# Optimization experiments

Hardware: AMD Instinct MI355X
Metric: run time of the kernel (lower is better)

## Reference

```python
import jax, jax.numpy as jnp
from jax import lax
import numpy as np

T, B, I, H = 512, 1024, 64, 64


def setup_inputs() -> dict:
    key = jax.random.key(0)
    k1, k2, k3, k4, k5 = jax.random.split(key, 5)
    s = 1.0 / np.sqrt(H)  # PyTorch GRU init scale
    X = jax.random.normal(k1, (T, B, I), dtype=jnp.float32)
    W_ih = jax.random.uniform(k2, (3 * H, I), jnp.float32, -s, s)
    W_hh = jax.random.uniform(k3, (3 * H, H), jnp.float32, -s, s)
    b_ih = jax.random.uniform(k4, (3 * H,), jnp.float32, -s, s)
    b_hh = jax.random.uniform(k5, (3 * H,), jnp.float32, -s, s)
    return {"X": X, "W_ih": W_ih, "W_hh": W_hh, "b_ih": b_ih, "b_hh": b_hh}


def reference(X, W_ih, W_hh, b_ih, b_hh):
    # Single-layer GRU, PyTorch semantics, gate order (r, z, n), h0 = 0.
    Hh = W_hh.shape[1]
    # Precompute input-side gate projections for all timesteps: [T, B, 3H]
    gates_x = jnp.einsum('tbi,gi->tbg', X, W_ih) + b_ih

    def step(h, gx):
        gh = h @ W_hh.T + b_hh  # [B, 3H]
        r = jax.nn.sigmoid(gx[:, :Hh] + gh[:, :Hh])
        z = jax.nn.sigmoid(gx[:, Hh:2 * Hh] + gh[:, Hh:2 * Hh])
        n = jnp.tanh(gx[:, 2 * Hh:] + r * gh[:, 2 * Hh:])
        h_new = (1.0 - z) * n + z * h
        return h_new, h_new

    h0 = jnp.zeros((X.shape[1], Hh), dtype=X.dtype)
    h_last, output = lax.scan(step, h0, gates_x)
    return output, h_last[None]  # ([T,B,H], [1,B,H])
```

## Files before the change

### kernel.cpp

```cpp
#include <hip/hip_runtime.h>


typedef _Float16 half8 __attribute__((ext_vector_type(8)));
typedef float    f32x4 __attribute__((ext_vector_type(4)));

#define T_STEPS 512
#define BATCH   1024

struct XBuf { float4 a0, a1, b0, b1; };

__device__ __forceinline__ half8 cvt8(const float4& a, const float4& b) {
    half8 h;
    h[0] = (_Float16)a.x; h[1] = (_Float16)a.y; h[2] = (_Float16)a.z; h[3] = (_Float16)a.w;
    h[4] = (_Float16)b.x; h[5] = (_Float16)b.y; h[6] = (_Float16)b.z; h[7] = (_Float16)b.w;
    return h;
}

__device__ __forceinline__ half8 loadw8(const float* p) {
    const float4* q = (const float4*)p;
    float4 a = q[0], b = q[1];
    return cvt8(a, b);
}

__device__ __forceinline__ void block_sync() {
    asm volatile("s_waitcnt lgkmcnt(0)" ::: "memory");
    __builtin_amdgcn_s_barrier();
    asm volatile("" ::: "memory");
}

#define MFMA16(A, B, C) __builtin_amdgcn_mfma_f32_16x16x32_f16((A), (B), (C), 0, 0, 0)

__global__ __launch_bounds__(256, 1)
void gru_mfma_kernel(const float* __restrict__ X,
                     const float* __restrict__ W_ih,
                     const float* __restrict__ W_hh,
                     const float* __restrict__ b_ih,
                     const float* __restrict__ b_hh,
                     float* __restrict__ out)
{
    const int tid   = threadIdx.x;
    const int w     = tid >> 6;
    const int l     = tid & 63;
    const int c     = l & 15;
    const int g4    = l >> 4;
    const int u     = w * 16 + c;
    const int row   = c;
    const int brow0 = blockIdx.x * 16;

    __shared__ __align__(16) _Float16 hbuf[2][16][72];

    const half8 Br0 = loadw8(W_ih + (u)       * 64 +  0 + 8 * g4);
    const half8 Br1 = loadw8(W_ih + (u)       * 64 + 32 + 8 * g4);
    const half8 Br2 = loadw8(W_hh + (u)       * 64 +  0 + 8 * g4);
    const half8 Br3 = loadw8(W_hh + (u)       * 64 + 32 + 8 * g4);
    const half8 Bz0 = loadw8(W_ih + (64 + u)  * 64 +  0 + 8 * g4);
    const half8 Bz1 = loadw8(W_ih + (64 + u)  * 64 + 32 + 8 * g4);
    const half8 Bz2 = loadw8(W_hh + (64 + u)  * 64 +  0 + 8 * g4);
    const half8 Bz3 = loadw8(W_hh + (64 + u)  * 64 + 32 + 8 * g4);
    const half8 Bnx0 = loadw8(W_ih + (128 + u) * 64 +  0 + 8 * g4);
    const half8 Bnx1 = loadw8(W_ih + (128 + u) * 64 + 32 + 8 * g4);
    const half8 Bnh0 = loadw8(W_hh + (128 + u) * 64 +  0 + 8 * g4);
    const half8 Bnh1 = loadw8(W_hh + (128 + u) * 64 + 32 + 8 * g4);

    const float rb  = b_ih[u]        + b_hh[u];
    const float zb  = b_ih[64 + u]   + b_hh[64 + u];
    const float nxb = b_ih[128 + u];
    const float nhb = b_hh[128 + u];

    f32x4 hp = {0.f, 0.f, 0.f, 0.f};

#define ISSUE_X(XB, T) do {                                                   \
        const float* px_ = X + ((T) * BATCH + brow0 + row) * 64 + 8 * g4;     \
        (XB).a0 = ((const float4*)px_)[0];                                    \
        (XB).a1 = ((const float4*)px_)[1];                                    \
        const float* py_ = px_ + 32;                                          \
        (XB).b0 = ((const float4*)py_)[0];                                    \
        (XB).b1 = ((const float4*)py_)[1];                                    \
    } while (0)

    XBuf xb0, xb1;
    ISSUE_X(xb0, 0);
    ISSUE_X(xb1, 1);

    for (int k = tid; k < 16 * 72; k += 256)
        ((_Float16*)hbuf)[k] = (_Float16)0.f;
    __syncthreads();

#define STEP(T, XB) do {                                                      \
        const int p_ = (T) & 1;                                               \
        const half8 hf0 = *(const half8*)&hbuf[p_][row][8 * g4];              \
        const half8 hf1 = *(const half8*)&hbuf[p_][row][32 + 8 * g4];         \
        const half8 xf0 = cvt8((XB).a0, (XB).a1);                             \
        const half8 xf1 = cvt8((XB).b0, (XB).b1);                             \
        { int tn_ = (T) + 2; if (tn_ > T_STEPS - 1) tn_ = T_STEPS - 1;        \
          ISSUE_X(XB, tn_); }                                                 \
        f32x4 cr  = {rb, rb, rb, rb};                                         \
        f32x4 cz  = {zb, zb, zb, zb};                                         \
        f32x4 cnx = {nxb, nxb, nxb, nxb};                                     \
        f32x4 cnh = {nhb, nhb, nhb, nhb};                                     \
        cr  = MFMA16(xf0, Br0, cr);   cr  = MFMA16(xf1, Br1, cr);             \
        cz  = MFMA16(xf0, Bz0, cz);   cz  = MFMA16(xf1, Bz1, cz);             \
        cnx = MFMA16(xf0, Bnx0, cnx); cnx = MFMA16(xf1, Bnx1, cnx);           \
        cr  = MFMA16(hf0, Br2, cr);   cr  = MFMA16(hf1, Br3, cr);             \
        cz  = MFMA16(hf0, Bz2, cz);   cz  = MFMA16(hf1, Bz3, cz);             \
        cnh = MFMA16(hf0, Bnh0, cnh); cnh = MFMA16(hf1, Bnh1, cnh);           \
        _Pragma("unroll")                                                     \
        for (int i = 0; i < 4; ++i) {                                         \
            const float rv = __builtin_amdgcn_rcpf(1.f + __expf(-cr[i]));     \
            const float zv = __builtin_amdgcn_rcpf(1.f + __expf(-cz[i]));     \
            const float npre = fmaf(rv, cnh[i], cnx[i]);                      \
            const float nv =                                                  \
                1.f - 2.f * __builtin_amdgcn_rcpf(1.f + __expf(2.f * npre));  \
            const float hn = fmaf(zv, hp[i] - nv, nv);                        \
            hp[i] = hn;                                                       \
            hbuf[p_ ^ 1][4 * g4 + i][u] = (_Float16)hn;                       \
            out[((T) * BATCH + brow0 + 4 * g4 + i) * 64 + u] = hn;            \
        }                                                                     \
        block_sync();                                                         \
    } while (0)

    #pragma unroll 1
    for (int t = 0; t < T_STEPS; t += 2) {
        STEP(t, xb0);
        STEP(t + 1, xb1);
    }

    #pragma unroll
    for (int i = 0; i < 4; ++i)
        out[T_STEPS * BATCH * 64 + (brow0 + 4 * g4 + i) * 64 + u] = hp[i];

#undef STEP
#undef ISSUE_X
}

extern "C" void kernel_launch(void* const* d_in, const int* in_sizes, int n_in,
                              void* d_out, int out_size, void* d_ws, size_t ws_size,
                              hipStream_t stream) {
    const float* X    = (const float*)d_in[0];
    const float* W_ih = (const float*)d_in[1];
    const float* W_hh = (const float*)d_in[2];
    const float* b_ih = (const float*)d_in[3];
    const float* b_hh = (const float*)d_in[4];
    float* out = (float*)d_out;

    dim3 grid(BATCH / 16);
    dim3 block(256);
    gru_mfma_kernel<<<grid, block, 0, stream>>>(X, W_ih, W_hh, b_ih, b_hh, out);
}
```

Baseline: 344.5 us.

## Software-pipeline input projection one step ahead of recurrent MFMA chain

The input-side gate MFMAs for timestep t+1 are now computed during step t, before the hidden-state MFMAs. This takes them off the serial h-dependent critical path, so each step only waits on six recurrent MFMAs plus the activation math. The next step's X tile is now converted one step earlier, which leaves less time to hide its global-load latency. It also keeps three more accumulator vectors live across the barrier.

Measured after the change: 438.9 us. 27.4% more time.

```diff
diff --git a/kernel.cpp b/kernel.cpp
--- a/kernel.cpp
+++ b/kernel.cpp
@@ -49,14 +49,14 @@
 
     __shared__ __align__(16) _Float16 hbuf[2][16][72];
 
-    const half8 Br0 = loadw8(W_ih + (u)       * 64 +  0 + 8 * g4);
-    const half8 Br1 = loadw8(W_ih + (u)       * 64 + 32 + 8 * g4);
-    const half8 Br2 = loadw8(W_hh + (u)       * 64 +  0 + 8 * g4);
-    const half8 Br3 = loadw8(W_hh + (u)       * 64 + 32 + 8 * g4);
-    const half8 Bz0 = loadw8(W_ih + (64 + u)  * 64 +  0 + 8 * g4);
-    const half8 Bz1 = loadw8(W_ih + (64 + u)  * 64 + 32 + 8 * g4);
-    const half8 Bz2 = loadw8(W_hh + (64 + u)  * 64 +  0 + 8 * g4);
-    const half8 Bz3 = loadw8(W_hh + (64 + u)  * 64 + 32 + 8 * g4);
+    const half8 Brx0 = loadw8(W_ih + (u)       * 64 +  0 + 8 * g4);
+    const half8 Brx1 = loadw8(W_ih + (u)       * 64 + 32 + 8 * g4);
+    const half8 Brh0 = loadw8(W_hh + (u)       * 64 +  0 + 8 * g4);
+    const half8 Brh1 = loadw8(W_hh + (u)       * 64 + 32 + 8 * g4);
+    const half8 Bzx0 = loadw8(W_ih + (64 + u)  * 64 +  0 + 8 * g4);
+    const half8 Bzx1 = loadw8(W_ih + (64 + u)  * 64 + 32 + 8 * g4);
+    const half8 Bzh0 = loadw8(W_hh + (64 + u)  * 64 +  0 + 8 * g4);
+    const half8 Bzh1 = loadw8(W_hh + (64 + u)  * 64 + 32 + 8 * g4);
     const half8 Bnx0 = loadw8(W_ih + (128 + u) * 64 +  0 + 8 * g4);
     const half8 Bnx1 = loadw8(W_ih + (128 + u) * 64 + 32 + 8 * g4);
     const half8 Bnh0 = loadw8(W_hh + (128 + u) * 64 +  0 + 8 * g4);
@@ -82,33 +82,51 @@
     ISSUE_X(xb0, 0);
     ISSUE_X(xb1, 1);
 
-    for (int k = tid; k < 16 * 72; k += 256)
+    for (int k = tid; k < 2 * 16 * 72; k += 256)
         ((_Float16*)hbuf)[k] = (_Float16)0.f;
+
+    f32x4 axr = {rb, rb, rb, rb};
+    f32x4 axz = {zb, zb, zb, zb};
+    f32x4 axn = {nxb, nxb, nxb, nxb};
+    {
+        const half8 x0 = cvt8(xb0.a0, xb0.a1);
+        const half8 x1 = cvt8(xb0.b0, xb0.b1);
+        axr = MFMA16(x0, Brx0, axr); axr = MFMA16(x1, Brx1, axr);
+        axz = MFMA16(x0, Bzx0, axz); axz = MFMA16(x1, Bzx1, axz);
+        axn = MFMA16(x0, Bnx0, axn); axn = MFMA16(x1, Bnx1, axn);
+    }
     __syncthreads();
 
-#define STEP(T, XB) do {                                                      \
+#define STEP(T, XA, XB) do {                                                  \
         const int p_ = (T) & 1;                                               \
+                 \
         const half8 hf0 = *(const half8*)&hbuf[p_][row][8 * g4];              \
         const half8 hf1 = *(const half8*)&hbuf[p_][row][32 + 8 * g4];         \
-        const half8 xf0 = cvt8((XB).a0, (XB).a1);                             \
-        const half8 xf1 = cvt8((XB).b0, (XB).b1);                             \
+           \
+        const half8 nxf0 = cvt8((XB).a0, (XB).a1);                            \
+        const half8 nxf1 = cvt8((XB).b0, (XB).b1);                            \
+        f32x4 naxr = {rb, rb, rb, rb};                                        \
+        f32x4 naxz = {zb, zb, zb, zb};                                        \
+        f32x4 naxn = {nxb, nxb, nxb, nxb};                                    \
+        naxr = MFMA16(nxf0, Brx0, naxr); naxr = MFMA16(nxf1, Brx1, naxr);     \
+        naxz = MFMA16(nxf0, Bzx0, naxz); naxz = MFMA16(nxf1, Bzx1, naxz);     \
+        naxn = MFMA16(nxf0, Bnx0, naxn); naxn = MFMA16(nxf1, Bnx1, naxn);     \
         { int tn_ = (T) + 2; if (tn_ > T_STEPS - 1) tn_ = T_STEPS - 1;        \
-          ISSUE_X(XB, tn_); }                                                 \
-        f32x4 cr  = {rb, rb, rb, rb};                                         \
-        f32x4 cz  = {zb, zb, zb, zb};                                         \
-        f32x4 cnx = {nxb, nxb, nxb, nxb};                                     \
-        f32x4 cnh = {nhb, nhb, nhb, nhb};                                     \
-        cr  = MFMA16(xf0, Br0, cr);   cr  = MFMA16(xf1, Br1, cr);             \
-        cz  = MFMA16(xf0, Bz0, cz);   cz  = MFMA16(xf1, Bz1, cz);             \
-        cnx = MFMA16(xf0, Bnx0, cnx); cnx = MFMA16(xf1, Bnx1, cnx);           \
-        cr  = MFMA16(hf0, Br2, cr);   cr  = MFMA16(hf1, Br3, cr);             \
-        cz  = MFMA16(hf0, Bz2, cz);   cz  = MFMA16(hf1, Bz3, cz);             \
-        cnh = MFMA16(hf0, Bnh0, cnh); cnh = MFMA16(hf1, Bnh1, cnh);           \
+          ISSUE_X(XA, tn_); }                                                 \
+                             \
+        f32x4 hr  = {0.f, 0.f, 0.f, 0.f};                                     \
+        f32x4 hz  = {0.f, 0.f, 0.f, 0.f};                                     \
+        f32x4 hnh = {nhb, nhb, nhb, nhb};                                     \
+        hr  = MFMA16(hf0, Brh0, hr);   hr  = MFMA16(hf1, Brh1, hr);           \
+        hz  = MFMA16(hf0, Bzh0, hz);   hz  = MFMA16(hf1, Bzh1, hz);           \
+        hnh = MFMA16(hf0, Bnh0, hnh);  hnh = MFMA16(hf1, Bnh1, hnh);          \
         _Pragma("unroll")                                                     \
         for (int i = 0; i < 4; ++i) {                                         \
-            const float rv = __builtin_amdgcn_rcpf(1.f + __expf(-cr[i]));     \
-            const float zv = __builtin_amdgcn_rcpf(1.f + __expf(-cz[i]));     \
-            const float npre = fmaf(rv, cnh[i], cnx[i]);                      \
+            const float crv = axr[i] + hr[i];                                 \
+            const float czv = axz[i] + hz[i];                                 \
+            const float rv = __builtin_amdgcn_rcpf(1.f + __expf(-crv));       \
+            const float zv = __builtin_amdgcn_rcpf(1.f + __expf(-czv));       \
+            const float npre = fmaf(rv, hnh[i], axn[i]);                      \
             const float nv =                                                  \
                 1.f - 2.f * __builtin_amdgcn_rcpf(1.f + __expf(2.f * npre));  \
             const float hn = fmaf(zv, hp[i] - nv, nv);                        \
@@ -116,13 +134,14 @@
             hbuf[p_ ^ 1][4 * g4 + i][u] = (_Float16)hn;                       \
             out[((T) * BATCH + brow0 + 4 * g4 + i) * 64 + u] = hn;            \
         }                                                                     \
+        axr = naxr; axz = naxz; axn = naxn;                                   \
         block_sync();                                                         \
     } while (0)
 
     #pragma unroll 1
     for (int t = 0; t < T_STEPS; t += 2) {
-        STEP(t, xb0);
-        STEP(t + 1, xb1);
+        STEP(t, xb0, xb1);
+        STEP(t + 1, xb1, xb0);
     }
 
     #pragma unroll
```

## Run each batch tile's GRU recurrence in one wave using cross-lane permutes

Applied to the files above, without the earlier changes.

Each 16-row batch tile is now handled by a single 64-lane wave instead of four waves. The hidden state is exchanged through ds_bpermute register shuffles rather than an LDS buffer and a block barrier at every timestep. The MFMA operands are swapped so the weights act as the A operand, and outputs are written as float4 vectors. This removes the per-step workgroup barrier and LDS round-trip. In exchange, each wave holds all 48 weight fragments in registers, issues four times as many MFMAs serially per step, and only 64 single-wave blocks run on the GPU.

Result: slower. 766.7 us (+122.6%).

```diff
diff --git a/kernel.cpp b/kernel.cpp
--- a/kernel.cpp
+++ b/kernel.cpp
@@ -1,8 +1,10 @@
 #include <hip/hip_runtime.h>
 
 
-typedef _Float16 half8 __attribute__((ext_vector_type(8)));
-typedef float    f32x4 __attribute__((ext_vector_type(4)));
+typedef _Float16 half8  __attribute__((ext_vector_type(8)));
+typedef __fp16   fp16x2 __attribute__((ext_vector_type(2)));
+typedef float    f32x4  __attribute__((ext_vector_type(4)));
+typedef int      i32x4  __attribute__((ext_vector_type(4)));
 
 #define T_STEPS 512
 #define BATCH   1024
@@ -18,116 +20,151 @@
 
 __device__ __forceinline__ half8 loadw8(const float* p) {
     const float4* q = (const float4*)p;
-    float4 a = q[0], b = q[1];
-    return cvt8(a, b);
+    return cvt8(q[0], q[1]);
 }
 
-__device__ __forceinline__ void block_sync() {
-    asm volatile("s_waitcnt lgkmcnt(0)" ::: "memory");
-    __builtin_amdgcn_s_barrier();
-    asm volatile("" ::: "memory");
+__device__ __forceinline__ int packrtz(float x, float y) {
+    fp16x2 p = __builtin_amdgcn_cvt_pkrtz(x, y);
+    return __builtin_bit_cast(int, p);
 }
 
 #define MFMA16(A, B, C) __builtin_amdgcn_mfma_f32_16x16x32_f16((A), (B), (C), 0, 0, 0)
 
-__global__ __launch_bounds__(256, 1)
-void gru_mfma_kernel(const float* __restrict__ X,
-                     const float* __restrict__ W_ih,
-                     const float* __restrict__ W_hh,
-                     const float* __restrict__ b_ih,
-                     const float* __restrict__ b_hh,
-                     float* __restrict__ out)
+__global__ __launch_bounds__(64, 1)
+void gru_1wave_kernel(const float* __restrict__ X,
+                      const float* __restrict__ W_ih,
+                      const float* __restrict__ W_hh,
+                      const float* __restrict__ b_ih,
+                      const float* __restrict__ b_hh,
+                      float* __restrict__ out)
 {
-    const int tid   = threadIdx.x;
-    const int w     = tid >> 6;
-    const int l     = tid & 63;
-    const int c     = l & 15;
+    const int l     = threadIdx.x;
+    const int b     = l & 15;
     const int g4    = l >> 4;
-    const int u     = w * 16 + c;
-    const int row   = c;
     const int brow0 = blockIdx.x * 16;
+    const bool hiHalf = (l >= 32);
 
-    __shared__ __align__(16) _Float16 hbuf[2][16][72];
+    const int idx0 = (b + 16 * ((g4 & 1) << 1)) << 2;
+    const int idx1 = idx0 + 64;
 
-    const half8 Br0 = loadw8(W_ih + (u)       * 64 +  0 + 8 * g4);
-    const half8 Br1 = loadw8(W_ih + (u)       * 64 + 32 + 8 * g4);
-    const half8 Br2 = loadw8(W_hh + (u)       * 64 +  0 + 8 * g4);
-    const half8 Br3 = loadw8(W_hh + (u)       * 64 + 32 + 8 * g4);
-    const half8 Bz0 = loadw8(W_ih + (64 + u)  * 64 +  0 + 8 * g4);
-    const half8 Bz1 = loadw8(W_ih + (64 + u)  * 64 + 32 + 8 * g4);
-    const half8 Bz2 = loadw8(W_hh + (64 + u)  * 64 +  0 + 8 * g4);
-    const half8 Bz3 = loadw8(W_hh + (64 + u)  * 64 + 32 + 8 * g4);
-    const half8 Bnx0 = loadw8(W_ih + (128 + u) * 64 +  0 + 8 * g4);
-    const half8 Bnx1 = loadw8(W_ih + (128 + u) * 64 + 32 + 8 * g4);
-    const half8 Bnh0 = loadw8(W_hh + (128 + u) * 64 +  0 + 8 * g4);
-    const half8 Bnh1 = loadw8(W_hh + (128 + u) * 64 + 32 + 8 * g4);
+    half8 Wih[3][4][2], Whh[3][4][2];
+    #pragma unroll
+    for (int g = 0; g < 3; ++g)
+        #pragma unroll
+        for (int ut = 0; ut < 4; ++ut)
+            #pragma unroll
+            for (int kk = 0; kk < 2; ++kk) {
+                const int row = g * 64 + 16 * ut + b;
+                Wih[g][ut][kk] = loadw8(W_ih + row * 64 + 32 * kk + 8 * g4);
+                Whh[g][ut][kk] = loadw8(W_hh + row * 64 + 32 * kk + 8 * g4);
+            }
 
-    const float rb  = b_ih[u]        + b_hh[u];
-    const float zb  = b_ih[64 + u]   + b_hh[64 + u];
-    const float nxb = b_ih[128 + u];
-    const float nhb = b_hh[128 + u];
+    f32x4 bR[4], bZ[4], bNX[4], bNH[4];
+    #pragma unroll
+    for (int ut = 0; ut < 4; ++ut) {
+        const int o = 16 * ut + 4 * g4;
+        const float4 i0 = *(const float4*)(b_ih + o);
+        const float4 h0 = *(const float4*)(b_hh + o);
+        const float4 i1 = *(const float4*)(b_ih + 64 + o);
+        const float4 h1 = *(const float4*)(b_hh + 64 + o);
+        const float4 i2 = *(const float4*)(b_ih + 128 + o);
+        const float4 h2 = *(const float4*)(b_hh + 128 + o);
+        bR[ut][0] = i0.x + h0.x; bR[ut][1] = i0.y + h0.y;
+        bR[ut][2] = i0.z + h0.z; bR[ut][3] = i0.w + h0.w;
+        bZ[ut][0] = i1.x + h1.x; bZ[ut][1] = i1.y + h1.y;
+        bZ[ut][2] = i1.z + h1.z; bZ[ut][3] = i1.w + h1.w;
+        bNX[ut][0] = i2.x; bNX[ut][1] = i2.y; bNX[ut][2] = i2.z; bNX[ut][3] = i2.w;
+        bNH[ut][0] = h2.x; bNH[ut][1] = h2.y; bNH[ut][2] = h2.z; bNH[ut][3] = h2.w;
+    }
 
-    f32x4 hp = {0.f, 0.f, 0.f, 0.f};
+    f32x4 hp[4] = {{0.f,0.f,0.f,0.f},{0.f,0.f,0.f,0.f},
+                   {0.f,0.f,0.f,0.f},{0.f,0.f,0.f,0.f}};
+    int hh[4][2] = {{0,0},{0,0},{0,0},{0,0}};
 
 #define ISSUE_X(XB, T) do {                                                   \
-        const float* px_ = X + ((T) * BATCH + brow0 + row) * 64 + 8 * g4;     \
+        const float* px_ = X + ((T) * BATCH + brow0 + b) * 64 + 8 * g4;       \
         (XB).a0 = ((const float4*)px_)[0];                                    \
         (XB).a1 = ((const float4*)px_)[1];                                    \
-        const float* py_ = px_ + 32;                                          \
-        (XB).b0 = ((const float4*)py_)[0];                                    \
-        (XB).b1 = ((const float4*)py_)[1];                                    \
+        (XB).b0 = ((const float4*)(px_ + 32))[0];                             \
+        (XB).b1 = ((const float4*)(px_ + 32))[1];                             \
     } while (0)
 
     XBuf xb0, xb1;
     ISSUE_X(xb0, 0);
     ISSUE_X(xb1, 1);
 
-    for (int k = tid; k < 16 * 72; k += 256)
-        ((_Float16*)hbuf)[k] = (_Float16)0.f;
-    __syncthreads();
-
-#define STEP(T, XB) do {                                                      \
-        const int p_ = (T) & 1;                                               \
-        const half8 hf0 = *(const half8*)&hbuf[p_][row][8 * g4];              \
-        const half8 hf1 = *(const half8*)&hbuf[p_][row][32 + 8 * g4];         \
-        const half8 xf0 = cvt8((XB).a0, (XB).a1);                             \
-        const half8 xf1 = cvt8((XB).b0, (XB).b1);                             \
+#define STEP(T, XA) do {                                                      \
+           \
+        i32x4 f0v, f1v;                                                       \
+        _Pragma("unroll")                                                     \
+        for (int jp = 0; jp < 4; ++jp) {                                      \
+            const int idx_ = (jp < 2) ? idx0 : idx1;                          \
+            const int lo0 = __builtin_amdgcn_ds_bpermute(idx_, hh[0][jp & 1]);\
+            const int hi0 = __builtin_amdgcn_ds_bpermute(idx_, hh[1][jp & 1]);\
+            const int lo1 = __builtin_amdgcn_ds_bpermute(idx_, hh[2][jp & 1]);\
+            const int hi1 = __builtin_amdgcn_ds_bpermute(idx_, hh[3][jp & 1]);\
+            f0v[jp] = hiHalf ? hi0 : lo0;                                     \
+            f1v[jp] = hiHalf ? hi1 : lo1;                                     \
+        }                                                                     \
+        const half8 Fh0 = __builtin_bit_cast(half8, f0v);                     \
+        const half8 Fh1 = __builtin_bit_cast(half8, f1v);                     \
+                         \
+        const half8 xf0 = cvt8((XA).a0, (XA).a1);                             \
+        const half8 xf1 = cvt8((XA).b0, (XA).b1);                             \
         { int tn_ = (T) + 2; if (tn_ > T_STEPS - 1) tn_ = T_STEPS - 1;        \
-          ISSUE_X(XB, tn_); }                                                 \
-        f32x4 cr  = {rb, rb, rb, rb};                                         \
-        f32x4 cz  = {zb, zb, zb, zb};                                         \
-        f32x4 cnx = {nxb, nxb, nxb, nxb};                                     \
-        f32x4 cnh = {nhb, nhb, nhb, nhb};                                     \
-        cr  = MFMA16(xf0, Br0, cr);   cr  = MFMA16(xf1, Br1, cr);             \
-        cz  = MFMA16(xf0, Bz0, cz);   cz  = MFMA16(xf1, Bz1, cz);             \
-        cnx = MFMA16(xf0, Bnx0, cnx); cnx = MFMA16(xf1, Bnx1, cnx);           \
-        cr  = MFMA16(hf0, Br2, cr);   cr  = MFMA16(hf1, Br3, cr);             \
-        cz  = MFMA16(hf0, Bz2, cz);   cz  = MFMA16(hf1, Bz3, cz);             \
-        cnh = MFMA16(hf0, Bnh0, cnh); cnh = MFMA16(hf1, Bnh1, cnh);           \
+          ISSUE_X(XA, tn_); }                                                 \
+            \
+        f32x4 aR[4], aZ[4], aNX[4], aNH[4];                                   \
         _Pragma("unroll")                                                     \
-        for (int i = 0; i < 4; ++i) {                                         \
-            const float rv = __builtin_amdgcn_rcpf(1.f + __expf(-cr[i]));     \
-            const float zv = __builtin_amdgcn_rcpf(1.f + __expf(-cz[i]));     \
-            const float npre = fmaf(rv, cnh[i], cnx[i]);                      \
-            const float nv =                                                  \
-                1.f - 2.f * __builtin_amdgcn_rcpf(1.f + __expf(2.f * npre));  \
-            const float hn = fmaf(zv, hp[i] - nv, nv);                        \
-            hp[i] = hn;                                                       \
-            hbuf[p_ ^ 1][4 * g4 + i][u] = (_Float16)hn;                       \
-            out[((T) * BATCH + brow0 + 4 * g4 + i) * 64 + u] = hn;            \
+        for (int ut = 0; ut < 4; ++ut) {                                      \
+            aR[ut]  = MFMA16(Wih[0][ut][0], xf0, bR[ut]);                     \
+            aR[ut]  = MFMA16(Wih[0][ut][1], xf1, aR[ut]);                     \
+            aZ[ut]  = MFMA16(Wih[1][ut][0], xf0, bZ[ut]);                     \
+            aZ[ut]  = MFMA16(Wih[1][ut][1], xf1, aZ[ut]);                     \
+            aNX[ut] = MFMA16(Wih[2][ut][0], xf0, bNX[ut]);                    \
+            aNX[ut] = MFMA16(Wih[2][ut][1], xf1, aNX[ut]);                    \
         }                                                                     \
-        block_sync();                                                         \
+        _Pragma("unroll")                                                     \
+        for (int ut = 0; ut < 4; ++ut) {                                      \
+            aR[ut]  = MFMA16(Whh[0][ut][0], Fh0, aR[ut]);                     \
+            aR[ut]  = MFMA16(Whh[0][ut][1], Fh1, aR[ut]);                     \
+            aZ[ut]  = MFMA16(Whh[1][ut][0], Fh0, aZ[ut]);                     \
+            aZ[ut]  = MFMA16(Whh[1][ut][1], Fh1, aZ[ut]);                     \
+            aNH[ut] = MFMA16(Whh[2][ut][0], Fh0, bNH[ut]);                    \
+            aNH[ut] = MFMA16(Whh[2][ut][1], Fh1, aNH[ut]);                    \
+        }                                                                     \
+                             \
+        _Pragma("unroll")                                                     \
+        for (int ut = 0; ut < 4; ++ut) {                                      \
+            f32x4 hn4;                                                        \
+            _Pragma("unroll")                                                 \
+            for (int i = 0; i < 4; ++i) {                                     \
+                const float rv = __builtin_amdgcn_rcpf(1.f + __expf(-aR[ut][i]));  \
+                const float zv = __builtin_amdgcn_rcpf(1.f + __expf(-aZ[ut][i]));  \
+                const float npre = fmaf(rv, aNH[ut][i], aNX[ut][i]);          \
+                const float nv =                                              \
+                    1.f - 2.f * __builtin_amdgcn_rcpf(1.f + __expf(2.f * npre));   \
+                const float hn = fmaf(zv, hp[ut][i] - nv, nv);                \
+                hp[ut][i] = hn;                                               \
+                hn4[i] = hn;                                                  \
+            }                                                                 \
+            hh[ut][0] = packrtz(hn4[0], hn4[1]);                              \
+            hh[ut][1] = packrtz(hn4[2], hn4[3]);                              \
+            *(f32x4*)(out + ((T) * BATCH + brow0 + b) * 64                    \
+                          + 16 * ut + 4 * g4) = hn4;                          \
+        }                                                                     \
     } while (0)
 
     #pragma unroll 1
     for (int t = 0; t < T_STEPS; t += 2) {
-        STEP(t, xb0);
+        STEP(t,     xb0);
         STEP(t + 1, xb1);
     }
 
     #pragma unroll
-    for (int i = 0; i < 4; ++i)
-        out[T_STEPS * BATCH * 64 + (brow0 + 4 * g4 + i) * 64 + u] = hp[i];
+    for (int ut = 0; ut < 4; ++ut)
+        *(f32x4*)(out + T_STEPS * BATCH * 64 + (brow0 + b) * 64
+                      + 16 * ut + 4 * g4) = hp[ut];
 
 #undef STEP
 #undef ISSUE_X
@@ -144,6 +181,6 @@
     float* out = (float*)d_out;
 
     dim3 grid(BATCH / 16);
-    dim3 block(256);
-    gru_mfma_kernel<<<grid, block, 0, stream>>>(X, W_ih, W_hh, b_ih, b_hh, out);
+    dim3 block(64);
+    gru_1wave_kernel<<<grid, block, 0, stream>>>(X, W_ih, W_hh, b_ih, b_hh, out);
 }
```

## Pair two batch tiles per block and fold exp scaling into weights

Applied to the files above, without the earlier changes.

Each block now runs two independent 16-row batch tiles across 8 waves, which halves the grid to 32 blocks of 512 threads. The log2e and negation factors are folded into the fp16 weights and biases so the gate activations use exp2 directly and skip a multiply. Activation conversion switches to packed cvt_pkrtz instructions. The cost is that both tiles share one block-wide barrier per step, the grid uses fewer CUs, and baking the scale into fp16 weights adds some rounding error.

New measurement: 652.5 us. 1.89x slower.

```diff
diff --git a/kernel.cpp b/kernel.cpp
--- a/kernel.cpp
+++ b/kernel.cpp
@@ -1,25 +1,38 @@
 #include <hip/hip_runtime.h>
 
 
-typedef _Float16 half8 __attribute__((ext_vector_type(8)));
-typedef float    f32x4 __attribute__((ext_vector_type(4)));
+typedef _Float16 half8  __attribute__((ext_vector_type(8)));
+typedef __fp16   fp16x2 __attribute__((ext_vector_type(2)));
+typedef float    f32x4  __attribute__((ext_vector_type(4)));
+typedef int      i32x4  __attribute__((ext_vector_type(4)));
 
 #define T_STEPS 512
 #define BATCH   1024
+#define LOG2E   1.4426950408889634f
 
 struct XBuf { float4 a0, a1, b0, b1; };
 
-__device__ __forceinline__ half8 cvt8(const float4& a, const float4& b) {
+__device__ __forceinline__ int pk2(float x, float y) {
+    fp16x2 p = __builtin_amdgcn_cvt_pkrtz(x, y);
+    return __builtin_bit_cast(int, p);
+}
+
+__device__ __forceinline__ half8 cvt8p(const float4& a, const float4& b) {
+    i32x4 v;
+    v[0] = pk2(a.x, a.y); v[1] = pk2(a.z, a.w);
+    v[2] = pk2(b.x, b.y); v[3] = pk2(b.z, b.w);
+    return __builtin_bit_cast(half8, v);
+}
+
+__device__ __forceinline__ half8 loadw8s(const float* p, float s) {
+    const float4* q = (const float4*)p;
+    float4 a = q[0], b = q[1];
+    a.x *= s; a.y *= s; a.z *= s; a.w *= s;
+    b.x *= s; b.y *= s; b.z *= s; b.w *= s;
     half8 h;
     h[0] = (_Float16)a.x; h[1] = (_Float16)a.y; h[2] = (_Float16)a.z; h[3] = (_Float16)a.w;
     h[4] = (_Float16)b.x; h[5] = (_Float16)b.y; h[6] = (_Float16)b.z; h[7] = (_Float16)b.w;
     return h;
-}
-
-__device__ __forceinline__ half8 loadw8(const float* p) {
-    const float4* q = (const float4*)p;
-    float4 a = q[0], b = q[1];
-    return cvt8(a, b);
 }
 
 __device__ __forceinline__ void block_sync() {
@@ -30,8 +43,8 @@
 
 #define MFMA16(A, B, C) __builtin_amdgcn_mfma_f32_16x16x32_f16((A), (B), (C), 0, 0, 0)
 
-__global__ __launch_bounds__(256, 1)
-void gru_mfma_kernel(const float* __restrict__ X,
+__global__ __launch_bounds__(512, 1)
+void gru_pair_kernel(const float* __restrict__ X,
                      const float* __restrict__ W_ih,
                      const float* __restrict__ W_hh,
                      const float* __restrict__ b_ih,
@@ -39,33 +52,38 @@
                      float* __restrict__ out)
 {
     const int tid   = threadIdx.x;
-    const int w     = tid >> 6;
+    const int wid   = tid >> 6;
+    const int wq    = wid & 3;
+    const int tile  = wid >> 2;
     const int l     = tid & 63;
     const int c     = l & 15;
     const int g4    = l >> 4;
-    const int u     = w * 16 + c;
+    const int u     = wq * 16 + c;
     const int row   = c;
-    const int brow0 = blockIdx.x * 16;
+    const int brow0 = blockIdx.x * 32 + tile * 16;
 
-    __shared__ __align__(16) _Float16 hbuf[2][16][72];
+    __shared__ __align__(16) _Float16 hbuf[2][2][16][72];
 
-    const half8 Br0 = loadw8(W_ih + (u)       * 64 +  0 + 8 * g4);
-    const half8 Br1 = loadw8(W_ih + (u)       * 64 + 32 + 8 * g4);
-    const half8 Br2 = loadw8(W_hh + (u)       * 64 +  0 + 8 * g4);
-    const half8 Br3 = loadw8(W_hh + (u)       * 64 + 32 + 8 * g4);
-    const half8 Bz0 = loadw8(W_ih + (64 + u)  * 64 +  0 + 8 * g4);
-    const half8 Bz1 = loadw8(W_ih + (64 + u)  * 64 + 32 + 8 * g4);
-    const half8 Bz2 = loadw8(W_hh + (64 + u)  * 64 +  0 + 8 * g4);
-    const half8 Bz3 = loadw8(W_hh + (64 + u)  * 64 + 32 + 8 * g4);
-    const half8 Bnx0 = loadw8(W_ih + (128 + u) * 64 +  0 + 8 * g4);
-    const half8 Bnx1 = loadw8(W_ih + (128 + u) * 64 + 32 + 8 * g4);
-    const half8 Bnh0 = loadw8(W_hh + (128 + u) * 64 +  0 + 8 * g4);
-    const half8 Bnh1 = loadw8(W_hh + (128 + u) * 64 + 32 + 8 * g4);
+    const float sRZ = -LOG2E;
+    const float sN  = 2.0f * LOG2E;
 
-    const float rb  = b_ih[u]        + b_hh[u];
-    const float zb  = b_ih[64 + u]   + b_hh[64 + u];
-    const float nxb = b_ih[128 + u];
-    const float nhb = b_hh[128 + u];
+    const half8 Brx0 = loadw8s(W_ih + (u)       * 64 +  0 + 8 * g4, sRZ);
+    const half8 Brx1 = loadw8s(W_ih + (u)       * 64 + 32 + 8 * g4, sRZ);
+    const half8 Brh0 = loadw8s(W_hh + (u)       * 64 +  0 + 8 * g4, sRZ);
+    const half8 Brh1 = loadw8s(W_hh + (u)       * 64 + 32 + 8 * g4, sRZ);
+    const half8 Bzx0 = loadw8s(W_ih + (64 + u)  * 64 +  0 + 8 * g4, sRZ);
+    const half8 Bzx1 = loadw8s(W_ih + (64 + u)  * 64 + 32 + 8 * g4, sRZ);
+    const half8 Bzh0 = loadw8s(W_hh + (64 + u)  * 64 +  0 + 8 * g4, sRZ);
+    const half8 Bzh1 = loadw8s(W_hh + (64 + u)  * 64 + 32 + 8 * g4, sRZ);
+    const half8 Bnx0 = loadw8s(W_ih + (128 + u) * 64 +  0 + 8 * g4, sN);
+    const half8 Bnx1 = loadw8s(W_ih + (128 + u) * 64 + 32 + 8 * g4, sN);
+    const half8 Bnh0 = loadw8s(W_hh + (128 + u) * 64 +  0 + 8 * g4, sN);
+    const half8 Bnh1 = loadw8s(W_hh + (128 + u) * 64 + 32 + 8 * g4, sN);
+
+    const float rb  = sRZ * (b_ih[u]      + b_hh[u]);
+    const float zb  = sRZ * (b_ih[64 + u] + b_hh[64 + u]);
+    const float nxb = sN * b_ih[128 + u];
+    const float nhb = sN * b_hh[128 + u];
 
     f32x4 hp = {0.f, 0.f, 0.f, 0.f};
 
@@ -73,47 +91,46 @@
         const float* px_ = X + ((T) * BATCH + brow0 + row) * 64 + 8 * g4;     \
         (XB).a0 = ((const float4*)px_)[0];                                    \
         (XB).a1 = ((const float4*)px_)[1];                                    \
-        const float* py_ = px_ + 32;                                          \
-        (XB).b0 = ((const float4*)py_)[0];                                    \
-        (XB).b1 = ((const float4*)py_)[1];                                    \
+        (XB).b0 = ((const float4*)(px_ + 32))[0];                             \
+        (XB).b1 = ((const float4*)(px_ + 32))[1];                             \
     } while (0)
 
     XBuf xb0, xb1;
     ISSUE_X(xb0, 0);
     ISSUE_X(xb1, 1);
 
-    for (int k = tid; k < 16 * 72; k += 256)
+    for (int k = tid; k < 2 * 2 * 16 * 72; k += 512)
         ((_Float16*)hbuf)[k] = (_Float16)0.f;
     __syncthreads();
 
 #define STEP(T, XB) do {                                                      \
         const int p_ = (T) & 1;                                               \
-        const half8 hf0 = *(const half8*)&hbuf[p_][row][8 * g4];              \
-        const half8 hf1 = *(const half8*)&hbuf[p_][row][32 + 8 * g4];         \
-        const half8 xf0 = cvt8((XB).a0, (XB).a1);                             \
-        const half8 xf1 = cvt8((XB).b0, (XB).b1);                             \
+        const half8 hf0 = *(const half8*)&hbuf[tile][p_][row][8 * g4];        \
+        const half8 hf1 = *(const half8*)&hbuf[tile][p_][row][32 + 8 * g4];   \
+        const half8 xf0 = cvt8p((XB).a0, (XB).a1);                            \
+        const half8 xf1 = cvt8p((XB).b0, (XB).b1);                            \
         { int tn_ = (T) + 2; if (tn_ > T_STEPS - 1) tn_ = T_STEPS - 1;        \
           ISSUE_X(XB, tn_); }                                                 \
         f32x4 cr  = {rb, rb, rb, rb};                                         \
         f32x4 cz  = {zb, zb, zb, zb};                                         \
         f32x4 cnx = {nxb, nxb, nxb, nxb};                                     \
         f32x4 cnh = {nhb, nhb, nhb, nhb};                                     \
-        cr  = MFMA16(xf0, Br0, cr);   cr  = MFMA16(xf1, Br1, cr);             \
-        cz  = MFMA16(xf0, Bz0, cz);   cz  = MFMA16(xf1, Bz1, cz);             \
+        cr  = MFMA16(xf0, Brx0, cr);  cr  = MFMA16(xf1, Brx1, cr);            \
+        cz  = MFMA16(xf0, Bzx0, cz);  cz  = MFMA16(xf1, Bzx1, cz);            \
         cnx = MFMA16(xf0, Bnx0, cnx); cnx = MFMA16(xf1, Bnx1, cnx);           \
-        cr  = MFMA16(hf0, Br2, cr);   cr  = MFMA16(hf1, Br3, cr);             \
-        cz  = MFMA16(hf0, Bz2, cz);   cz  = MFMA16(hf1, Bz3, cz);             \
+        cr  = MFMA16(hf0, Brh0, cr);  cr  = MFMA16(hf1, Brh1, cr);            \
+        cz  = MFMA16(hf0, Bzh0, cz);  cz  = MFMA16(hf1, Bzh1, cz);            \
         cnh = MFMA16(hf0, Bnh0, cnh); cnh = MFMA16(hf1, Bnh1, cnh);           \
         _Pragma("unroll")                                                     \
         for (int i = 0; i < 4; ++i) {                                         \
-            const float rv = __builtin_amdgcn_rcpf(1.f + __expf(-cr[i]));     \
-            const float zv = __builtin_amdgcn_rcpf(1.f + __expf(-cz[i]));     \
+            const float rv = __builtin_amdgcn_rcpf(1.f + exp2f(cr[i]));       \
+            const float zv = __builtin_amdgcn_rcpf(1.f + exp2f(cz[i]));       \
             const float npre = fmaf(rv, cnh[i], cnx[i]);                      \
-            const float nv =                                                  \
-                1.f - 2.f * __builtin_amdgcn_rcpf(1.f + __expf(2.f * npre));  \
+            const float e  = exp2f(npre);                                     \
+            const float nv = 1.f - 2.f * __builtin_amdgcn_rcpf(e + 1.f);      \
             const float hn = fmaf(zv, hp[i] - nv, nv);                        \
             hp[i] = hn;                                                       \
-            hbuf[p_ ^ 1][4 * g4 + i][u] = (_Float16)hn;                       \
+            hbuf[tile][p_ ^ 1][4 * g4 + i][u] = (_Float16)hn;                 \
             out[((T) * BATCH + brow0 + 4 * g4 + i) * 64 + u] = hn;            \
         }                                                                     \
         block_sync();                                                         \
@@ -143,7 +160,7 @@
     const float* b_hh = (const float*)d_in[4];
     float* out = (float*)d_out;
 
-    dim3 grid(BATCH / 16);
-    dim3 block(256);
-    gru_mfma_kernel<<<grid, block, 0, stream>>>(X, W_ih, W_hh, b_ih, b_hh, out);
+    dim3 grid(BATCH / 32);
+    dim3 block(512);
+    gru_pair_kernel<<<grid, block, 0, stream>>>(X, W_ih, W_hh, b_ih, b_hh, out);
 }
```
